# Performance work log

Hardware: AMD Instinct MI355X
Metric: run time of the kernel (lower is better)

## Reference

```python
import jax, jax.numpy as jnp
import numpy as np

NUM_LEVELS = 4
RADIUS = 3


def bilinear_sample(feat, coords):
    """feat: (B,H,W,C); coords: (B, ..., 2) with [x,y] order. Returns (B, ..., C).
    Matches the original: corner indices are clipped FIRST, then weights are
    computed from the clipped indices."""
    B, H, W, C = feat.shape
    x = coords[..., 0]
    y = coords[..., 1]
    x0 = jnp.clip(jnp.floor(x).astype(jnp.int32), 0, W - 1)
    x1 = jnp.clip(jnp.floor(x).astype(jnp.int32) + 1, 0, W - 1)
    y0 = jnp.clip(jnp.floor(y).astype(jnp.int32), 0, H - 1)
    y1 = jnp.clip(jnp.floor(y).astype(jnp.int32) + 1, 0, H - 1)
    x0f = x0.astype(jnp.float32); x1f = x1.astype(jnp.float32)
    y0f = y0.astype(jnp.float32); y1f = y1.astype(jnp.float32)
    wa = (x1f - x) * (y1f - y)
    wb = (x1f - x) * (y - y0f)
    wc = (x - x0f) * (y1f - y)
    wd = (x - x0f) * (y - y0f)
    bidx = jnp.arange(B).reshape((B,) + (1,) * (coords.ndim - 2))
    Ia = feat[bidx, y0, x0]
    Ib = feat[bidx, y1, x0]
    Ic = feat[bidx, y0, x1]
    Id = feat[bidx, y1, x1]
    return wa[..., None] * Ia + wb[..., None] * Ib + wc[..., None] * Ic + wd[..., None] * Id


def _normalize(v):
    return v / (jnp.linalg.norm(v, axis=-1, keepdims=True) + 1e-06)


def setup_inputs() -> dict:
    key = jax.random.key(0)
    k1, k2, k3, k4 = jax.random.split(key, 4)
    B, H, W, C, N = 2, 64, 64, 256, 4096
    fmap1 = jax.random.normal(k1, (B, H, W, C), dtype=jnp.float32)
    fmap2 = jax.random.normal(k2, (B, H, W, C), dtype=jnp.float32)
    scale = jnp.array([W - 1, H - 1], dtype=jnp.float32)
    coords1 = jax.random.uniform(k3, (B, N, 2), dtype=jnp.float32) * scale
    coords2 = jax.random.uniform(k4, (B, N, 2), dtype=jnp.float32) * scale
    return {"fmap1": fmap1, "fmap2": fmap2, "coords1": coords1, "coords2": coords2}


def reference(fmap1, fmap2, coords1, coords2):
    r = RADIUS
    B, H, W, C = fmap1.shape
    feat1 = _normalize(bilinear_sample(fmap1, coords1))  # (B,N,C)
    # Offset grid, dy-major then dx (matches the original nested loops),
    # stored as [dx, dy] to match `coords + [dx, dy]`.
    d = jnp.arange(-r, r + 1, dtype=jnp.float32)
    dyg, dxg = jnp.meshgrid(d, d, indexing='ij')
    offs = jnp.stack([dxg.ravel(), dyg.ravel()], axis=-1)  # (K,2), K=(2r+1)^2
    corr_list = []
    fmap2_l = fmap2  # cascaded pyramid, as in the original
    for level in range(NUM_LEVELS):
        if level > 0:
            fmap2_l = jax.image.resize(
                fmap2_l, (B, H // 2 ** level, W // 2 ** level, C), method='bilinear')
        H_l, W_l = fmap2_l.shape[1], fmap2_l.shape[2]
        f2n = _normalize(fmap2_l)
        scale = 2.0 ** level
        c = coords2[:, :, None, :] / scale + offs[None, None, :, :]  # (B,N,K,2)
        c = jnp.clip(c, jnp.zeros(2, jnp.float32),
                     jnp.array([W_l - 1, H_l - 1], dtype=jnp.float32))
        feat2 = bilinear_sample(f2n, c)  # (B,N,K,C)
        corr_list.append(jnp.einsum('bnc,bnkc->bnk', feat1, feat2))
    return jnp.concatenate(corr_list, axis=-1)  # (B,N,NUM_LEVELS*K)
```

## Files before the change

### kernel.cpp

```cpp
#include <hip/hip_runtime.h>
#include <math.h>

#define NB   2
#define H0   64
#define W0   64
#define NC   256
#define NPTS 4096
#define NLVL 4
#define NK   49

__device__ __forceinline__ float wave_reduce_sum(float v) {
    for (int m = 32; m >= 1; m >>= 1)
        v += __shfl_xor(v, m, 64);
    return v;
}

__device__ __forceinline__ float wave_reduce_max(float v) {
    for (int m = 32; m >= 1; m >>= 1)
        v = fmaxf(v, __shfl_xor(v, m, 64));
    return v;
}

__device__ __forceinline__ int dot4i(unsigned a, unsigned b, int c) {
#if defined(__has_builtin)
#if __has_builtin(__builtin_amdgcn_sdot4)
    return __builtin_amdgcn_sdot4((int)a, (int)b, c, false);
#else
    c += (((int)(a << 24)) >> 24) * (((int)(b << 24)) >> 24);
    c += (((int)(a << 16)) >> 24) * (((int)(b << 16)) >> 24);
    c += (((int)(a <<  8)) >> 24) * (((int)(b <<  8)) >> 24);
    c += (((int)a) >> 24)         * (((int)b) >> 24);
    return c;
#endif
#else
    c += (((int)(a << 24)) >> 24) * (((int)(b << 24)) >> 24);
    c += (((int)(a << 16)) >> 24) * (((int)(b << 16)) >> 24);
    c += (((int)(a <<  8)) >> 24) * (((int)(b <<  8)) >> 24);
    c += (((int)a) >> 24)         * (((int)b) >> 24);
    return c;
#endif
}

__device__ __forceinline__ void quant_store(float nx, float ny, float nz, float nw,
                                            unsigned char* __restrict__ qout,
                                            size_t pixIdx,
                                            float* __restrict__ sout, int lane) {
    float m = fmaxf(fmaxf(fabsf(nx), fabsf(ny)), fmaxf(fabsf(nz), fabsf(nw)));
    float M = wave_reduce_max(m);
    float s = (M > 0.f) ? 127.f / M : 0.f;
    int qx = __float2int_rn(nx * s), qy = __float2int_rn(ny * s);
    int qz = __float2int_rn(nz * s), qw = __float2int_rn(nw * s);
    unsigned p = (qx & 0xff) | ((qy & 0xff) << 8) | ((qz & 0xff) << 16) | ((qw & 0xff) << 24);
    ((unsigned*)(qout + pixIdx * NC))[lane] = p;
    if (lane == 0) sout[pixIdx] = (M > 0.f) ? M / 127.f : 0.f;
}

__device__ __forceinline__ void down_norm(const float* __restrict__ in,
                                          float* __restrict__ raw_out,
                                          unsigned char* __restrict__ qout,
                                          float* __restrict__ sout,
                                          int Hi, int Wi, int wid, int lane) {
    int Ho = Hi >> 1, Wo = Wi >> 1;
    int b = wid / (Ho * Wo);
    int rem = wid - b * (Ho * Wo);
    int yo = rem / Wo, xo = rem - yo * Wo;
    float wy[4], wx[4]; int ty[4], tx[4];
    float sy = 0.f, sx = 0.f;
    for (int j = 0; j < 4; ++j) {
        float w = (j == 0 || j == 3) ? 1.f : 3.f;
        int yi = 2 * yo - 1 + j;
        float wyj = (yi >= 0 && yi < Hi) ? w : 0.f;
        ty[j] = min(max(yi, 0), Hi - 1); wy[j] = wyj; sy += wyj;
        int xi = 2 * xo - 1 + j;
        float wxj = (xi >= 0 && xi < Wi) ? w : 0.f;
        tx[j] = min(max(xi, 0), Wi - 1); wx[j] = wxj; sx += wxj;
    }
    float inv_s = 1.f / (sy * sx);
    float ax = 0.f, ay = 0.f, az = 0.f, aw = 0.f;
    const float4* basep = (const float4*)(in + (size_t)b * Hi * Wi * NC);
    for (int jy = 0; jy < 4; ++jy) {
        if (wy[jy] == 0.f) continue;
        for (int jx = 0; jx < 4; ++jx) {
            float w = wy[jy] * wx[jx];
            if (w == 0.f) continue;
            float4 v = basep[(ty[jy] * Wi + tx[jx]) * (NC / 4) + lane];
            ax += w * v.x; ay += w * v.y; az += w * v.z; aw += w * v.w;
        }
    }
    ax *= inv_s; ay *= inv_s; az *= inv_s; aw *= inv_s;
    float ss = wave_reduce_sum(ax * ax + ay * ay + az * az + aw * aw);
    float inv = 1.f / (sqrtf(ss) + 1e-6f);
    size_t po = (size_t)b * Ho * Wo + (size_t)yo * Wo + xo;
    if (raw_out) {
        float4 r; r.x = ax; r.y = ay; r.z = az; r.w = aw;
        ((float4*)raw_out)[po * (NC / 4) + lane] = r;
    }
    quant_store(ax * inv, ay * inv, az * inv, aw * inv, qout, po, sout, lane);
}

__device__ __forceinline__ void down3_composed(const float* __restrict__ raw1,
                                               unsigned char* __restrict__ qout,
                                               float* __restrict__ sout,
                                               int wid, int lane) {
    int b = wid / 64;
    int rem = wid - b * 64;
    int yo = rem >> 3, xo = rem & 7;
    float Wt[2][10]; int base[2];
    for (int d = 0; d < 2; ++d) {
        int o = d ? xo : yo;
        base[d] = 4 * o - 3;
        float W[10];
        for (int k = 0; k < 10; ++k) W[k] = 0.f;
        float S2 = 0.f;
        for (int j = 0; j < 4; ++j) {
            int yj = 2 * o - 1 + j;
            if (yj < 0 || yj >= 16) continue;
            float wj = (j == 0 || j == 3) ? 1.f : 3.f;
            S2 += wj;
            int yi0 = 2 * yj - 1;
            float wi[4], s1 = 0.f;
            for (int i2 = 0; i2 < 4; ++i2) {
                int yi = yi0 + i2;
                wi[i2] = (yi >= 0 && yi < 32) ? ((i2 == 0 || i2 == 3) ? 1.f : 3.f) : 0.f;
                s1 += wi[i2];
            }
            float sc = wj / s1;
            for (int i2 = 0; i2 < 4; ++i2)
                if (wi[i2] > 0.f) W[yi0 + i2 - base[d]] += wi[i2] * sc;
        }
        float invS = 1.f / S2;
        for (int k = 0; k < 10; ++k) Wt[d][k] = W[k] * invS;
    }
    float ax = 0.f, ay = 0.f, az = 0.f, aw = 0.f;
    const float4* basep = (const float4*)(raw1 + (size_t)b * 32 * 32 * NC);
    for (int ky = 0; ky < 10; ++ky) {
        float wy = Wt[0][ky];
        if (wy == 0.f) continue;
        int yi = base[0] + ky;
        for (int kx = 0; kx < 10; ++kx) {
            float wx = Wt[1][kx];
            if (wx == 0.f) continue;
            int xi = base[1] + kx;
            float4 v = basep[(yi * 32 + xi) * (NC / 4) + lane];
            float wgt = wy * wx;
            ax += wgt * v.x; ay += wgt * v.y; az += wgt * v.z; aw += wgt * v.w;
        }
    }
    float ss = wave_reduce_sum(ax * ax + ay * ay + az * az + aw * aw);
    float inv = 1.f / (sqrtf(ss) + 1e-6f);
    size_t po = (size_t)b * 64 + yo * 8 + xo;
    quant_store(ax * inv, ay * inv, az * inv, aw * inv, qout, po, sout, lane);
}

__global__ __launch_bounds__(256)
void pre_kernel(const float* __restrict__ fmap1,
                const float* __restrict__ fmap2,
                const float* __restrict__ coords1,
                unsigned char* __restrict__ f1q, float* __restrict__ fsc,
                unsigned char* __restrict__ q0,  float* __restrict__ s0,
                float* __restrict__ raw1,
                unsigned char* __restrict__ q1,  float* __restrict__ s1) {
    int blk  = blockIdx.x;
    int wv   = threadIdx.x >> 6;
    int lane = threadIdx.x & 63;
    if (blk < 2048) {
        int pt = blk * 4 + wv;
        int b = pt / NPTS;
        float x = coords1[pt * 2 + 0];
        float y = coords1[pt * 2 + 1];
        int x0 = min(max((int)floorf(x), 0), W0 - 1);
        int y0 = min(max((int)floorf(y), 0), H0 - 1);
        int x1 = min(x0 + 1, W0 - 1);
        int y1 = min(y0 + 1, H0 - 1);
        float wxh = x - (float)x0, wxl = (float)x1 - x;
        float wyh = y - (float)y0, wyl = (float)y1 - y;
        float wa = wxl * wyl, wb = wxl * wyh, wc = wxh * wyl, wd = wxh * wyh;
        const float4* base = (const float4*)(fmap1 + (size_t)b * H0 * W0 * NC);
        float4 Ia = base[(y0 * W0 + x0) * (NC / 4) + lane];
        float4 Ib = base[(y1 * W0 + x0) * (NC / 4) + lane];
        float4 Ic = base[(y0 * W0 + x1) * (NC / 4) + lane];
        float4 Id = base[(y1 * W0 + x1) * (NC / 4) + lane];
        float vx = wa * Ia.x + wb * Ib.x + wc * Ic.x + wd * Id.x;
        float vy = wa * Ia.y + wb * Ib.y + wc * Ic.y + wd * Id.y;
        float vz = wa * Ia.z + wb * Ib.z + wc * Ic.z + wd * Id.z;
        float vw = wa * Ia.w + wb * Ib.w + wc * Ic.w + wd * Id.w;
        float ss = wave_reduce_sum(vx * vx + vy * vy + vz * vz + vw * vw);
        float inv = 1.0f / (sqrtf(ss) + 1e-6f);
        quant_store(vx * inv, vy * inv, vz * inv, vw * inv, f1q, pt, fsc, lane);
    } else if (blk < 4096) {
        int p = (blk - 2048) * 4 + wv;
        float4 v = ((const float4*)fmap2)[(size_t)p * (NC / 4) + lane];
        float ss = wave_reduce_sum(v.x * v.x + v.y * v.y + v.z * v.z + v.w * v.w);
        float inv = 1.0f / (sqrtf(ss) + 1e-6f);
        quant_store(v.x * inv, v.y * inv, v.z * inv, v.w * inv, q0, p, s0, lane);
    } else {
        int wid = (blk - 4096) * 4 + wv;
        down_norm(fmap2, raw1, q1, s1, H0, W0, wid, lane);
    }
}

__global__ __launch_bounds__(256)
void small_kernel(const float* __restrict__ raw1,
                  unsigned char* __restrict__ q2, float* __restrict__ s2,
                  unsigned char* __restrict__ q3, float* __restrict__ s3) {
    int blk  = blockIdx.x;
    int wv   = threadIdx.x >> 6;
    int lane = threadIdx.x & 63;
    if (blk < 128) {
        int wid = blk * 4 + wv;
        down_norm(raw1, (float*)nullptr, q2, s2, 32, 32, wid, lane);
    } else {
        int wid = (blk - 128) * 4 + wv;
        down3_composed(raw1, q3, s3, wid, lane);
    }
}

__device__ __forceinline__ int tile_dot(const uint4* buf, const uint4* a4) {
    int ac = 0;
#pragma unroll
    for (int s = 0; s < 4; ++s) {
        uint4 u = buf[s], av = a4[s];
        ac = dot4i(av.x, u.x, ac);
        ac = dot4i(av.y, u.y, ac);
        ac = dot4i(av.z, u.z, ac);
        ac = dot4i(av.w, u.w, ac);
    }
    return ac;
}

__global__ __launch_bounds__(256)
void corr_kernel(const unsigned char* __restrict__ f1q,
                 const float* __restrict__ fsc,
                 const float* __restrict__ coords2,
                 const unsigned char* __restrict__ q0, const float* __restrict__ s0,
                 const unsigned char* __restrict__ q1, const float* __restrict__ s1,
                 const unsigned char* __restrict__ q2, const float* __restrict__ s2,
                 const unsigned char* __restrict__ q3, const float* __restrict__ s3,
                 float* __restrict__ out) {
    __shared__ float Ds[NLVL][64];
    int pt = blockIdx.x;
    int b  = pt / NPTS;
    int t  = threadIdx.x;

    int w    = t >> 6;
    int lane = t & 63;
    int Wl = W0 >> w, Hl = H0 >> w;
    float invs = 1.0f / (float)(1 << w);
    float cx = coords2[pt * 2 + 0] * invs;
    float cy = coords2[pt * 2 + 1] * invs;
    int ix = (int)floorf(cx), iy = (int)floorf(cy);

    const unsigned char* f2q = (w == 0) ? q0 : (w == 1) ? q1 : (w == 2) ? q2 : q3;
    const float*         f2s = (w == 0) ? s0 : (w == 1) ? s1 : (w == 2) ? s2 : s3;

    int cg = lane & 3;
    int pq = lane >> 2;

    const uint4* pixp[4];
    float sb[4];
#pragma unroll
    for (int i = 0; i < 4; ++i) {
        int p  = i * 16 + pq;
        int jx = p & 7, jy = p >> 3;
        int px = min(max(ix - 3 + jx, 0), Wl - 1);
        int py = min(max(iy - 3 + jy, 0), Hl - 1);
        int idx = (b * Hl + py) * Wl + px;
        pixp[i] = (const uint4*)(f2q + (size_t)idx * NC);
        sb[i]   = f2s[idx];
    }
    float sa = fsc[pt];

    const uint4* f1p = (const uint4*)(f1q + (size_t)pt * NC);
    uint4 a4[4];
#pragma unroll
    for (int s = 0; s < 4; ++s) a4[s] = f1p[s * 4 + cg];

    uint4 b0[4], b1[4];
#pragma unroll
    for (int s = 0; s < 4; ++s) b0[s] = pixp[0][s * 4 + cg];
#pragma unroll
    for (int s = 0; s < 4; ++s) b1[s] = pixp[1][s * 4 + cg];

    int ac;
#define EMIT(i, ac_) {                                                   \
        int r = (ac_);                                                   \
        r += __shfl_xor(r, 1, 64);                                       \
        r += __shfl_xor(r, 2, 64);                                       \
        if (cg == 0) Ds[w][(i) * 16 + pq] = (float)r * sa * sb[i];       \
    }
    ac = tile_dot(b0, a4);
#pragma unroll
    for (int s = 0; s < 4; ++s) b0[s] = pixp[2][s * 4 + cg];
    EMIT(0, ac);
    ac = tile_dot(b1, a4);
#pragma unroll
    for (int s = 0; s < 4; ++s) b1[s] = pixp[3][s * 4 + cg];
    EMIT(1, ac);
    ac = tile_dot(b0, a4);
    EMIT(2, ac);
    ac = tile_dot(b1, a4);
    EMIT(3, ac);
#undef EMIT
    __syncthreads();

    if (lane < NK) {
        int tyk = lane / 7, txk = lane % 7;
        float dx = (float)(txk - 3), dy = (float)(tyk - 3);
        float x = fminf(fmaxf(cx + dx, 0.f), (float)(Wl - 1));
        float y = fminf(fmaxf(cy + dy, 0.f), (float)(Hl - 1));
        int x0 = (int)floorf(x);
        int y0 = (int)floorf(y);
        int x1 = min(x0 + 1, Wl - 1);
        int y1 = min(y0 + 1, Hl - 1);
        float wxh = x - (float)x0, wxl = (float)x1 - x;
        float wyh = y - (float)y0, wyl = (float)y1 - y;
        int sx0 = min(max(x0 - ix + 3, 0), 7);
        int sx1 = min(max(x1 - ix + 3, 0), 7);
        int sy0 = min(max(y0 - iy + 3, 0), 7);
        int sy1 = min(max(y1 - iy + 3, 0), 7);
        float v = wxl * wyl * Ds[w][sy0 * 8 + sx0]
                + wxl * wyh * Ds[w][sy1 * 8 + sx0]
                + wxh * wyl * Ds[w][sy0 * 8 + sx1]
                + wxh * wyh * Ds[w][sy1 * 8 + sx1];
        out[(size_t)pt * (NLVL * NK) + w * NK + lane] = v;
    }
}

extern "C" void kernel_launch(void* const* d_in, const int* in_sizes, int n_in,
                              void* d_out, int out_size, void* d_ws, size_t ws_size,
                              hipStream_t stream) {
    const float* fmap1   = (const float*)d_in[0];
    const float* fmap2   = (const float*)d_in[1];
    const float* coords1 = (const float*)d_in[2];
    const float* coords2 = (const float*)d_in[3];
    float* out = (float*)d_out;
    float* ws  = (float*)d_ws;

    float*         raw1 = ws;
    unsigned char* f1q  = (unsigned char*)(ws + 524288);
    float*         fsc  = ws + 1048576;
    unsigned char* q0   = (unsigned char*)(ws + 1056768);
    float*         s0   = ws + 1581056;
    unsigned char* q1   = (unsigned char*)(ws + 1589248);
    float*         s1   = ws + 1720320;
    unsigned char* q2   = (unsigned char*)(ws + 1722368);
    float*         s2   = ws + 1755136;
    unsigned char* q3   = (unsigned char*)(ws + 1755648);
    float*         s3   = ws + 1763840;

    pre_kernel<<<4608, 256, 0, stream>>>(fmap1, fmap2, coords1,
                                         f1q, fsc, q0, s0, raw1, q1, s1);
    small_kernel<<<160, 256, 0, stream>>>(raw1, q2, s2, q3, s3);
    corr_kernel<<<NB * NPTS, 256, 0, stream>>>(f1q, fsc, coords2,
                                               q0, s0, q1, s1, q2, s2, q3, s3, out);
}
```

Measured before the change: 132.8 us.

## Split small-level downsampling across block waves and hoist corr gathers

small_kernel now assigns one 256-thread block per output pixel instead of one wave, with the four waves splitting the tap rows and combining partial sums through shared memory before normalizing and quantizing. The grid grows from 160 to 640 blocks, which raises parallelism for this latency-bound tiny kernel. corr_kernel also issues all four pixel-tile loads up front instead of double-buffering two at a time, which exposes more memory-level parallelism at the cost of extra registers. The scale loads are moved after the tile loads.

```diff
diff --git a/kernel.cpp b/kernel.cpp
--- a/kernel.cpp
+++ b/kernel.cpp
@@ -95,60 +95,6 @@
         float4 r; r.x = ax; r.y = ay; r.z = az; r.w = aw;
         ((float4*)raw_out)[po * (NC / 4) + lane] = r;
     }
-    quant_store(ax * inv, ay * inv, az * inv, aw * inv, qout, po, sout, lane);
-}
-
-__device__ __forceinline__ void down3_composed(const float* __restrict__ raw1,
-                                               unsigned char* __restrict__ qout,
-                                               float* __restrict__ sout,
-                                               int wid, int lane) {
-    int b = wid / 64;
-    int rem = wid - b * 64;
-    int yo = rem >> 3, xo = rem & 7;
-    float Wt[2][10]; int base[2];
-    for (int d = 0; d < 2; ++d) {
-        int o = d ? xo : yo;
-        base[d] = 4 * o - 3;
-        float W[10];
-        for (int k = 0; k < 10; ++k) W[k] = 0.f;
-        float S2 = 0.f;
-        for (int j = 0; j < 4; ++j) {
-            int yj = 2 * o - 1 + j;
-            if (yj < 0 || yj >= 16) continue;
-            float wj = (j == 0 || j == 3) ? 1.f : 3.f;
-            S2 += wj;
-            int yi0 = 2 * yj - 1;
-            float wi[4], s1 = 0.f;
-            for (int i2 = 0; i2 < 4; ++i2) {
-                int yi = yi0 + i2;
-                wi[i2] = (yi >= 0 && yi < 32) ? ((i2 == 0 || i2 == 3) ? 1.f : 3.f) : 0.f;
-                s1 += wi[i2];
-            }
-            float sc = wj / s1;
-            for (int i2 = 0; i2 < 4; ++i2)
-                if (wi[i2] > 0.f) W[yi0 + i2 - base[d]] += wi[i2] * sc;
-        }
-        float invS = 1.f / S2;
-        for (int k = 0; k < 10; ++k) Wt[d][k] = W[k] * invS;
-    }
-    float ax = 0.f, ay = 0.f, az = 0.f, aw = 0.f;
-    const float4* basep = (const float4*)(raw1 + (size_t)b * 32 * 32 * NC);
-    for (int ky = 0; ky < 10; ++ky) {
-        float wy = Wt[0][ky];
-        if (wy == 0.f) continue;
-        int yi = base[0] + ky;
-        for (int kx = 0; kx < 10; ++kx) {
-            float wx = Wt[1][kx];
-            if (wx == 0.f) continue;
-            int xi = base[1] + kx;
-            float4 v = basep[(yi * 32 + xi) * (NC / 4) + lane];
-            float wgt = wy * wx;
-            ax += wgt * v.x; ay += wgt * v.y; az += wgt * v.z; aw += wgt * v.w;
-        }
-    }
-    float ss = wave_reduce_sum(ax * ax + ay * ay + az * az + aw * aw);
-    float inv = 1.f / (sqrtf(ss) + 1e-6f);
-    size_t po = (size_t)b * 64 + yo * 8 + xo;
     quant_store(ax * inv, ay * inv, az * inv, aw * inv, qout, po, sout, lane);
 }
 
@@ -203,15 +149,102 @@
 void small_kernel(const float* __restrict__ raw1,
                   unsigned char* __restrict__ q2, float* __restrict__ s2,
                   unsigned char* __restrict__ q3, float* __restrict__ s3) {
+    __shared__ float4 part[4][64];
     int blk  = blockIdx.x;
     int wv   = threadIdx.x >> 6;
     int lane = threadIdx.x & 63;
-    if (blk < 128) {
-        int wid = blk * 4 + wv;
-        down_norm(raw1, (float*)nullptr, q2, s2, 32, 32, wid, lane);
+    float ax = 0.f, ay = 0.f, az = 0.f, aw = 0.f;
+    unsigned char* qout; float* sout; size_t po;
+
+    if (blk < 512) {
+        int b = blk >> 8, rem = blk & 255;
+        int yo = rem >> 4, xo = rem & 15;
+        float wy[4], wx[4]; int ty[4], tx[4];
+        float sy = 0.f, sx = 0.f;
+#pragma unroll
+        for (int j = 0; j < 4; ++j) {
+            float w = (j == 0 || j == 3) ? 1.f : 3.f;
+            int yi = 2 * yo - 1 + j;
+            float wyj = (yi >= 0 && yi < 32) ? w : 0.f;
+            ty[j] = min(max(yi, 0), 31); wy[j] = wyj; sy += wyj;
+            int xi = 2 * xo - 1 + j;
+            float wxj = (xi >= 0 && xi < 32) ? w : 0.f;
+            tx[j] = min(max(xi, 0), 31); wx[j] = wxj; sx += wxj;
+        }
+        float inv_s = 1.f / (sy * sx);
+        const float4* basep = (const float4*)(raw1 + (size_t)b * 32 * 32 * NC);
+        int jy = wv;
+        if (wy[jy] != 0.f) {
+#pragma unroll
+            for (int jx = 0; jx < 4; ++jx) {
+                float w = wy[jy] * wx[jx] * inv_s;
+                if (wx[jx] == 0.f) continue;
+                float4 v = basep[(ty[jy] * 32 + tx[jx]) * (NC / 4) + lane];
+                ax += w * v.x; ay += w * v.y; az += w * v.z; aw += w * v.w;
+            }
+        }
+        qout = q2; sout = s2; po = (size_t)b * 256 + yo * 16 + xo;
     } else {
-        int wid = (blk - 128) * 4 + wv;
-        down3_composed(raw1, q3, s3, wid, lane);
+        int wid = blk - 512;
+        int b = wid >> 6, rem = wid & 63;
+        int yo = rem >> 3, xo = rem & 7;
+        float Wt[2][10]; int base[2];
+        for (int d = 0; d < 2; ++d) {
+            int o = d ? xo : yo;
+            base[d] = 4 * o - 3;
+            float W[10];
+            for (int k = 0; k < 10; ++k) W[k] = 0.f;
+            float S2 = 0.f;
+            for (int j = 0; j < 4; ++j) {
+                int yj = 2 * o - 1 + j;
+                if (yj < 0 || yj >= 16) continue;
+                float wj = (j == 0 || j == 3) ? 1.f : 3.f;
+                S2 += wj;
+                int yi0 = 2 * yj - 1;
+                float wi[4], s1v = 0.f;
+                for (int i2 = 0; i2 < 4; ++i2) {
+                    int yi = yi0 + i2;
+                    wi[i2] = (yi >= 0 && yi < 32) ? ((i2 == 0 || i2 == 3) ? 1.f : 3.f) : 0.f;
+                    s1v += wi[i2];
+                }
+                float sc = wj / s1v;
+                for (int i2 = 0; i2 < 4; ++i2)
+                    if (wi[i2] > 0.f) W[yi0 + i2 - base[d]] += wi[i2] * sc;
+            }
+            float invS = 1.f / S2;
+            for (int k = 0; k < 10; ++k) Wt[d][k] = W[k] * invS;
+        }
+        const float4* basep = (const float4*)(raw1 + (size_t)b * 32 * 32 * NC);
+        for (int ky = wv; ky < 10; ky += 4) {
+            float wyk = Wt[0][ky];
+            if (wyk == 0.f) continue;
+            int yi = base[0] + ky;
+#pragma unroll
+            for (int kx = 0; kx < 10; ++kx) {
+                float wxk = Wt[1][kx];
+                if (wxk == 0.f) continue;
+                int xi = base[1] + kx;
+                float wgt = wyk * wxk;
+                float4 v = basep[(yi * 32 + xi) * (NC / 4) + lane];
+                ax += wgt * v.x; ay += wgt * v.y; az += wgt * v.z; aw += wgt * v.w;
+            }
+        }
+        qout = q3; sout = s3; po = (size_t)b * 64 + yo * 8 + xo;
+    }
+
+    float4 pr; pr.x = ax; pr.y = ay; pr.z = az; pr.w = aw;
+    part[wv][lane] = pr;
+    __syncthreads();
+    if (wv == 0) {
+        float4 p0 = part[0][lane], p1 = part[1][lane];
+        float4 p2 = part[2][lane], p3 = part[3][lane];
+        ax = p0.x + p1.x + p2.x + p3.x;
+        ay = p0.y + p1.y + p2.y + p3.y;
+        az = p0.z + p1.z + p2.z + p3.z;
+        aw = p0.w + p1.w + p2.w + p3.w;
+        float ss = wave_reduce_sum(ax * ax + ay * ay + az * az + aw * aw);
+        float inv = 1.f / (sqrtf(ss) + 1e-6f);
+        quant_store(ax * inv, ay * inv, az * inv, aw * inv, qout, po, sout, lane);
     }
 }
 
@@ -257,50 +290,41 @@
     int pq = lane >> 2;
 
     const uint4* pixp[4];
-    float sb[4];
+    int pidx[4];
 #pragma unroll
     for (int i = 0; i < 4; ++i) {
         int p  = i * 16 + pq;
         int jx = p & 7, jy = p >> 3;
         int px = min(max(ix - 3 + jx, 0), Wl - 1);
         int py = min(max(iy - 3 + jy, 0), Hl - 1);
-        int idx = (b * Hl + py) * Wl + px;
-        pixp[i] = (const uint4*)(f2q + (size_t)idx * NC);
-        sb[i]   = f2s[idx];
-    }
-    float sa = fsc[pt];
+        pidx[i] = (b * Hl + py) * Wl + px;
+        pixp[i] = (const uint4*)(f2q + (size_t)pidx[i] * NC);
+    }
+
+    uint4 bufs[4][4];
+#pragma unroll
+    for (int i = 0; i < 4; ++i)
+#pragma unroll
+        for (int s = 0; s < 4; ++s)
+            bufs[i][s] = pixp[i][s * 4 + cg];
 
     const uint4* f1p = (const uint4*)(f1q + (size_t)pt * NC);
     uint4 a4[4];
 #pragma unroll
     for (int s = 0; s < 4; ++s) a4[s] = f1p[s * 4 + cg];
 
-    uint4 b0[4], b1[4];
-#pragma unroll
-    for (int s = 0; s < 4; ++s) b0[s] = pixp[0][s * 4 + cg];
-#pragma unroll
-    for (int s = 0; s < 4; ++s) b1[s] = pixp[1][s * 4 + cg];
-
-    int ac;
-#define EMIT(i, ac_) {                                                   \
-        int r = (ac_);                                                   \
-        r += __shfl_xor(r, 1, 64);                                       \
-        r += __shfl_xor(r, 2, 64);                                       \
-        if (cg == 0) Ds[w][(i) * 16 + pq] = (float)r * sa * sb[i];       \
-    }
-    ac = tile_dot(b0, a4);
-#pragma unroll
-    for (int s = 0; s < 4; ++s) b0[s] = pixp[2][s * 4 + cg];
-    EMIT(0, ac);
-    ac = tile_dot(b1, a4);
-#pragma unroll
-    for (int s = 0; s < 4; ++s) b1[s] = pixp[3][s * 4 + cg];
-    EMIT(1, ac);
-    ac = tile_dot(b0, a4);
-    EMIT(2, ac);
-    ac = tile_dot(b1, a4);
-    EMIT(3, ac);
-#undef EMIT
+    float sb[4];
+#pragma unroll
+    for (int i = 0; i < 4; ++i) sb[i] = f2s[pidx[i]];
+    float sa = fsc[pt];
+
+#pragma unroll
+    for (int i = 0; i < 4; ++i) {
+        int r = tile_dot(bufs[i], a4);
+        r += __shfl_xor(r, 1, 64);
+        r += __shfl_xor(r, 2, 64);
+        if (cg == 0) Ds[w][i * 16 + pq] = (float)r * sa * sb[i];
+    }
     __syncthreads();
 
     if (lane < NK) {
@@ -350,7 +374,7 @@
 
     pre_kernel<<<4608, 256, 0, stream>>>(fmap1, fmap2, coords1,
                                          f1q, fsc, q0, s0, raw1, q1, s1);
-    small_kernel<<<160, 256, 0, stream>>>(raw1, q2, s2, q3, s3);
+    small_kernel<<<640, 256, 0, stream>>>(raw1, q2, s2, q3, s3);
     corr_kernel<<<NB * NPTS, 256, 0, stream>>>(f1q, fsc, coords2,
                                                q0, s0, q1, s1, q2, s2, q3, s3, out);
 }
```

Result: faster. 110.7 us (-16.6%).
